# Kernel tuning notes

Hardware: AMD Instinct MI355X
Metric: run time of the kernel (lower is better)

## Reference

```python
import jax, jax.numpy as jnp
import numpy as np

N6 = 524288          # nodes at depth 6 (full-octree batch of 2)
N5 = N6 // 8         # 65536 nodes at depth 5
N4 = N5 // 8         # 8192 nodes at depth 4
EPS = 1e-5           # torch BatchNorm1d default eps


def _pool(x):
    # octree_max_pool on a full octree: 8 contiguous children -> parent max
    n, c = x.shape
    return jnp.max(x.reshape(n // 8, 8, c), axis=1)


def _up(x):
    # octree_upsample on a full octree: each parent broadcast to its 8 children
    return jnp.repeat(x, 8, axis=0)


def _conv1x1_bn_relu(x, w, g, b):
    # Conv1x1 (Linear, no bias) + BatchNorm1d (training-mode batch stats) + ReLU
    y = x @ w                              # [N, Cout]
    m = jnp.mean(y, axis=0)
    v = jnp.var(y, axis=0)                 # biased variance, as in torch BN
    y = (y - m) * jax.lax.rsqrt(v + EPS) * g + b
    return jax.nn.relu(y)


def setup_inputs() -> dict:
    key = jax.random.key(0)
    ks = jax.random.split(key, 8)
    s = 0.02
    return {
        "data0": jax.random.normal(ks[0], (N6, 96), jnp.float32),
        "data1": jax.random.normal(ks[1], (N5, 192), jnp.float32),
        "w01": jax.random.normal(ks[2], (96, 192), jnp.float32) * s,
        "g01": jnp.ones((192,), jnp.float32),
        "b01": jnp.zeros((192,), jnp.float32),
        "w02": jax.random.normal(ks[3], (96, 384), jnp.float32) * s,
        "g02": jnp.ones((384,), jnp.float32),
        "b02": jnp.zeros((384,), jnp.float32),
        "w10": jax.random.normal(ks[4], (192, 96), jnp.float32) * s,
        "g10": jnp.ones((96,), jnp.float32),
        "b10": jnp.zeros((96,), jnp.float32),
        "w12": jax.random.normal(ks[5], (192, 384), jnp.float32) * s,
        "g12": jnp.ones((384,), jnp.float32),
        "b12": jnp.zeros((384,), jnp.float32),
        "depth": 6,
    }


def reference(data0, data1, w01, g01, b01, w02, g02, b02,
              w10, g10, b10, w12, g12, b12, depth):
    # channels = [96, 192, 384]; data0 at depth, data1 at depth-1.
    # out[j] = sum_i TransFunc(channels[i]->channels[j])(data[i], depth-i -> depth-j)
    # j=0 (depth, 96ch):   identity(data0) + upsample(conv10(data1))
    out0 = data0 + _up(_conv1x1_bn_relu(data1, w10, g10, b10))
    # j=1 (depth-1, 192ch): conv01(pool(data0)) + identity(data1)
    p0 = _pool(data0)                      # [N5, 96]
    out1 = _conv1x1_bn_relu(p0, w01, g01, b01) + data1
    # j=2 (depth-2, 384ch): conv02(pool^2(data0)) + conv12(pool(data1))
    out2 = (_conv1x1_bn_relu(_pool(p0), w02, g02, b02)
            + _conv1x1_bn_relu(_pool(data1), w12, g12, b12))
    return (out0, out1, out2)
```

## Files before the change

### kernel.cpp

```cpp
#include <hip/hip_runtime.h>

typedef unsigned short u16;
typedef __attribute__((ext_vector_type(8))) short short8;
typedef __attribute__((ext_vector_type(4))) float f4;
typedef __attribute__((ext_vector_type(4))) unsigned short u16x4;

#define CN6 524288
#define CN5 65536
#define CN4 8192

__device__ inline u16 f2bf(float f){
  unsigned u = __float_as_uint(f);
  return (u16)((u + 0x7FFFu + ((u >> 16) & 1u)) >> 16);
}
__device__ inline float bf2f(u16 h){ return __uint_as_float(((unsigned)h) << 16); }

__device__ inline f4 nt_load4(const float* p){
  return __builtin_nontemporal_load(reinterpret_cast<const f4*>(p));
}
__device__ inline void nt_store4(float* p, f4 v){
  __builtin_nontemporal_store(v, reinterpret_cast<f4*>(p));
}


__global__ __launch_bounds__(256) void k_prep(const float* __restrict__ w10, const float* __restrict__ w01,
                                              const float* __restrict__ w02, const float* __restrict__ w12,
                                              u16* __restrict__ wT10, u16* __restrict__ wT01,
                                              u16* __restrict__ wT02, u16* __restrict__ wT12,
                                              float* __restrict__ stats){
  int i = blockIdx.x * 256 + threadIdx.x;
  if (i < 2112) stats[i] = 0.f;
  if (i < 18432){ int j = i / 192, k = i - j * 192; wT10[i] = f2bf(w10[k * 96 + j]); }
  else if (i < 36864){ int e = i - 18432; int j = e / 96, k = e - j * 96; wT01[e] = f2bf(w01[k * 192 + j]); }
  else if (i < 73728){ int e = i - 36864; int j = e / 96, k = e - j * 96; wT02[e] = f2bf(w02[k * 384 + j]); }
  else if (i < 147456){ int e = i - 73728; int j = e / 192, k = e - j * 192; wT12[e] = f2bf(w12[k * 384 + j]); }
}

__global__ __launch_bounds__(256) void k_gemm10p(const float* __restrict__ d1, const u16* __restrict__ wT10,
                                                 u16* __restrict__ y10, u16* __restrict__ p1){
  __shared__ u16 sm[32 * 200];
  int tid = threadIdx.x, bid = blockIdx.x;

  if (tid < 96){
    int p = tid / 24, c8 = tid - p * 24;
    f4 v0[8], v1[8];
    #pragma unroll
    for (int r = 0; r < 8; r++){
      const float* src = d1 + ((size_t)bid * 32 + p * 8 + r) * 192 + c8 * 8;
      v0[r] = *reinterpret_cast<const f4*>(src);
      v1[r] = *reinterpret_cast<const f4*>(src + 4);
    }
    float mx[8];
    #pragma unroll
    for (int q = 0; q < 4; q++){ mx[q] = v0[0][q]; mx[4 + q] = v1[0][q]; }
    #pragma unroll
    for (int r = 0; r < 8; r++){
      short8 h;
      #pragma unroll
      for (int q = 0; q < 4; q++){
        h[q]     = (short)f2bf(v0[r][q]);
        h[4 + q] = (short)f2bf(v1[r][q]);
        if (r){ mx[q] = fmaxf(mx[q], v0[r][q]); mx[4 + q] = fmaxf(mx[4 + q], v1[r][q]); }
      }
      *reinterpret_cast<short8*>(&sm[(p * 8 + r) * 200 + c8 * 8]) = h;
    }
    short8 hp;
    #pragma unroll
    for (int q = 0; q < 8; q++) hp[q] = (short)f2bf(mx[q]);
    *reinterpret_cast<short8*>(p1 + ((size_t)bid * 4 + p) * 192 + c8 * 8) = hp;
  }
  __syncthreads();

  int lane = tid & 63, wave = tid >> 6;
  int colb = lane & 15;
  int k0 = (lane >> 4) * 8, rgrp = (lane >> 4) * 4;
  int arowl = (wave & 1) * 16 + colb;
  int jbase = (wave >> 1) * 3;
  short8 xf[6];
  #pragma unroll
  for (int s = 0; s < 6; s++) xf[s] = *reinterpret_cast<short8*>(&sm[arowl * 200 + s * 32 + k0]);

  size_t xrow = (size_t)bid * 32 + arowl;
  #pragma unroll
  for (int jj = 0; jj < 3; jj++){
    int j = jbase + jj;
    f4 acc = {0.f, 0.f, 0.f, 0.f};
    const u16* wr = wT10 + (size_t)(j * 16 + colb) * 192 + k0;
    #pragma unroll
    for (int s = 0; s < 6; s++)
      acc = __builtin_amdgcn_mfma_f32_16x16x32_bf16(*reinterpret_cast<const short8*>(wr + s * 32), xf[s], acc, 0, 0, 0);
    u16x4 h;
    #pragma unroll
    for (int r = 0; r < 4; r++) h[r] = f2bf(acc[r]);
    *reinterpret_cast<u16x4*>(y10 + xrow * 96 + j * 16 + rgrp) = h;
  }
}

__global__ __launch_bounds__(192) void k_stats10(const u16* __restrict__ y10, float* __restrict__ stats){
  __shared__ float ls[96], lq[96];
  int tid = threadIdx.x, bid = blockIdx.x;
  if (tid < 96){ ls[tid] = 0.f; lq[tid] = 0.f; }
  __syncthreads();
  int c8 = tid % 12, rl = tid / 12;
  float s1[8], s2[8];
  #pragma unroll
  for (int q = 0; q < 8; q++){ s1[q] = 0.f; s2[q] = 0.f; }
  for (int it = 0; it < 32; it++){
    size_t row = (size_t)bid * 512 + it * 16 + rl;
    short8 h = *reinterpret_cast<const short8*>(y10 + row * 96 + c8 * 8);
    #pragma unroll
    for (int q = 0; q < 8; q++){
      float v = bf2f((u16)h[q]);
      s1[q] += v; s2[q] += v * v;
    }
  }
  #pragma unroll
  for (int q = 0; q < 8; q++){
    atomicAdd(&ls[c8 * 8 + q], s1[q]);
    atomicAdd(&lq[c8 * 8 + q], s2[q]);
  }
  __syncthreads();
  if (tid < 96){ atomicAdd(&stats[tid], ls[tid]); atomicAdd(&stats[1056 + tid], lq[tid]); }
}

__global__ __launch_bounds__(256) void k_out0(const float* __restrict__ d0, const u16* __restrict__ y10,
                                              const float* __restrict__ stats,
                                              const float* __restrict__ g10, const float* __restrict__ b10,
                                              float* __restrict__ out0, u16* __restrict__ p0, u16* __restrict__ p00){
  __shared__ float yv[8][96];
  __shared__ float sd[64][100];
  __shared__ float sp[8][96];
  int tid = threadIdx.x, gp = blockIdx.x;

  if (tid < 192){
    int p = tid / 24, c4 = tid - p * 24;
    u16x4 yb = *reinterpret_cast<const u16x4*>(y10 + ((size_t)gp * 8 + p) * 96 + c4 * 4);
    f4 o;
    #pragma unroll
    for (int q = 0; q < 4; q++){
      int c = c4 * 4 + q;
      float m = stats[c] * (1.f / 65536.f);
      float vv = stats[1056 + c] * (1.f / 65536.f) - m * m;
      float a = g10[c] * rsqrtf(vv + 1e-5f);
      float cc = b10[c] - m * a;
      o[q] = fmaxf(bf2f((u16)yb[q]) * a + cc, 0.f);
    }
    *reinterpret_cast<f4*>(&yv[p][c4 * 4]) = o;
  }
  __syncthreads();

  const float* dsrc = d0 + (size_t)gp * 6144;
  float* ddst = out0 + (size_t)gp * 6144;
  f4 v[6];
  #pragma unroll
  for (int i = 0; i < 6; i++) v[i] = nt_load4(dsrc + (i * 256 + tid) * 4);
  #pragma unroll
  for (int i = 0; i < 6; i++){
    int idx = i * 256 + tid;
    int row = idx / 24, c4 = idx - row * 24;
    f4 y = *reinterpret_cast<f4*>(&yv[row >> 3][c4 * 4]);
    f4 o;
    #pragma unroll
    for (int q = 0; q < 4; q++) o[q] = v[i][q] + y[q];
    nt_store4(ddst + idx * 4, o);
    *reinterpret_cast<f4*>(&sd[row][c4 * 4]) = v[i];
  }
  __syncthreads();

  if (tid < 192){
    int p = tid / 24, c4 = tid - p * 24;
    f4 m = *reinterpret_cast<f4*>(&sd[p * 8][c4 * 4]);
    #pragma unroll
    for (int r = 1; r < 8; r++){
      f4 x = *reinterpret_cast<f4*>(&sd[p * 8 + r][c4 * 4]);
      #pragma unroll
      for (int q = 0; q < 4; q++) m[q] = fmaxf(m[q], x[q]);
    }
    u16x4 h;
    #pragma unroll
    for (int q = 0; q < 4; q++) h[q] = f2bf(m[q]);
    *reinterpret_cast<u16x4*>(p0 + ((size_t)gp * 8 + p) * 96 + c4 * 4) = h;
    *reinterpret_cast<f4*>(&sp[p][c4 * 4]) = m;
  }
  __syncthreads();
  if (tid < 24){
    f4 m = *reinterpret_cast<f4*>(&sp[0][tid * 4]);
    #pragma unroll
    for (int pp = 1; pp < 8; pp++){
      f4 x = *reinterpret_cast<f4*>(&sp[pp][tid * 4]);
      #pragma unroll
      for (int q = 0; q < 4; q++) m[q] = fmaxf(m[q], x[q]);
    }
    u16x4 h;
    #pragma unroll
    for (int q = 0; q < 4; q++) h[q] = f2bf(m[q]);
    *reinterpret_cast<u16x4*>(p00 + (size_t)gp * 96 + tid * 4) = h;
  }
}

template<int Ci, int Co>
__device__ __forceinline__ void stats_body(const u16* __restrict__ x, const u16* __restrict__ wT,
                                           float* __restrict__ sum, float* __restrict__ sq,
                                           int bid, float* ls, float* lq){
  int tid = threadIdx.x;
  for (int t = tid; t < Co; t += 256){ ls[t] = 0.f; lq[t] = 0.f; }
  __syncthreads();
  int lane = tid & 63, wave = tid >> 6;
  int arow = bid * 64 + wave * 16 + (lane & 15);
  int k0 = (lane >> 4) * 8;
  constexpr int KS = Ci / 32;
  short8 af[KS];
  const u16* xr = x + (size_t)arow * Ci + k0;
  #pragma unroll
  for (int s = 0; s < KS; s++) af[s] = *reinterpret_cast<const short8*>(xr + s * 32);
  int colb = lane & 15;
  #pragma unroll 4
  for (int j = 0; j < Co / 16; j++){
    int col = j * 16 + colb;
    f4 acc = {0.f, 0.f, 0.f, 0.f};
    const u16* wr = wT + (size_t)col * Ci + k0;
    #pragma unroll
    for (int s = 0; s < KS; s++)
      acc = __builtin_amdgcn_mfma_f32_16x16x32_bf16(af[s], *reinterpret_cast<const short8*>(wr + s * 32), acc, 0, 0, 0);
    float s1 = acc[0] + acc[1] + acc[2] + acc[3];
    float s2 = acc[0]*acc[0] + acc[1]*acc[1] + acc[2]*acc[2] + acc[3]*acc[3];
    atomicAdd(&ls[col], s1);
    atomicAdd(&lq[col], s2);
  }
  __syncthreads();
  for (int t = tid; t < Co; t += 256){ atomicAdd(&sum[t], ls[t]); atomicAdd(&sq[t], lq[t]); }
}

__global__ __launch_bounds__(256) void k_statsAll(const u16* __restrict__ p0, const u16* __restrict__ p00,
                                                  const u16* __restrict__ p1,
                                                  const u16* __restrict__ wT01, const u16* __restrict__ wT02,
                                                  const u16* __restrict__ wT12, float* __restrict__ stats){
  __shared__ float ls[384], lq[384];
  int bid = blockIdx.x;
  if (bid < 1024)      stats_body<96, 192>(p0,  wT01, stats + 96,  stats + 1056 + 96,  bid,        ls, lq);
  else if (bid < 1152) stats_body<96, 384>(p00, wT02, stats + 288, stats + 1056 + 288, bid - 1024, ls, lq);
  else                 stats_body<192,384>(p1,  wT12, stats + 672, stats + 1056 + 672, bid - 1152, ls, lq);
}

__global__ __launch_bounds__(256) void k_out1(const u16* __restrict__ p0, const u16* __restrict__ wT01,
                                              const float* __restrict__ d1, const float* __restrict__ stats,
                                              const float* __restrict__ g01, const float* __restrict__ b01,
                                              float* __restrict__ out1){
  __shared__ float aL[192], cL[192];
  __shared__ float so[32 * 196];
  int tid = threadIdx.x, bid = blockIdx.x;
  if (tid < 192){
    float m = stats[96 + tid] * (1.f / 65536.f);
    float v = stats[1056 + 96 + tid] * (1.f / 65536.f) - m * m;
    float a = g01[tid] * rsqrtf(v + 1e-5f);
    aL[tid] = a; cL[tid] = b01[tid] - m * a;
  }
  __syncthreads();
  int lane = tid & 63, wave = tid >> 6;
  int colb = lane & 15;
  int k0 = (lane >> 4) * 8, rgrp = (lane >> 4) * 4;
  int rowl = (wave & 1) * 16 + colb;
  int jbase = (wave >> 1) * 6;
  short8 xf[3];
  const u16* xr = p0 + ((size_t)bid * 32 + rowl) * 96 + k0;
  #pragma unroll
  for (int s = 0; s < 3; s++) xf[s] = *reinterpret_cast<const short8*>(xr + s * 32);
  #pragma unroll
  for (int jj = 0; jj < 6; jj++){
    int j = jbase + jj;
    int ch0 = j * 16 + rgrp;
    f4 acc = {0.f, 0.f, 0.f, 0.f};
    const u16* wr = wT01 + (size_t)(j * 16 + colb) * 96 + k0;
    #pragma unroll
    for (int s = 0; s < 3; s++)
      acc = __builtin_amdgcn_mfma_f32_16x16x32_bf16(*reinterpret_cast<const short8*>(wr + s * 32), xf[s], acc, 0, 0, 0);
    f4 o;
    #pragma unroll
    for (int r = 0; r < 4; r++){
      int ch = ch0 + r;
      o[r] = fmaxf(acc[r] * aL[ch] + cL[ch], 0.f);
    }
    *reinterpret_cast<f4*>(&so[rowl * 196 + ch0]) = o;
  }
  __syncthreads();
  const float* d1b = d1 + (size_t)bid * 32 * 192;
  float* o1b = out1 + (size_t)bid * 32 * 192;
  #pragma unroll
  for (int i = 0; i < 6; i++){
    int idx = i * 256 + tid;
    int rl = idx / 48, c4i = idx % 48;
    f4 y = *reinterpret_cast<f4*>(&so[rl * 196 + c4i * 4]);
    int off = rl * 192 + c4i * 4;
    f4 g = nt_load4(d1b + off);
    f4 o;
    #pragma unroll
    for (int q = 0; q < 4; q++) o[q] = y[q] + g[q];
    nt_store4(o1b + off, o);
  }
}

__global__ __launch_bounds__(256) void k_out2(const u16* __restrict__ p00, const u16* __restrict__ p1,
                                              const u16* __restrict__ wT02, const u16* __restrict__ wT12,
                                              const float* __restrict__ stats,
                                              const float* __restrict__ g02, const float* __restrict__ b02,
                                              const float* __restrict__ g12, const float* __restrict__ b12,
                                              float* __restrict__ out2){
  __shared__ float a2[384], c2[384], a1[384], c1[384];
  __shared__ float so[32 * 392];
  int tid = threadIdx.x, bid = blockIdx.x;
  for (int t = tid; t < 384; t += 256){
    float m = stats[288 + t] * (1.f / 8192.f);
    float v = stats[1056 + 288 + t] * (1.f / 8192.f) - m * m;
    float a = g02[t] * rsqrtf(v + 1e-5f);
    a2[t] = a; c2[t] = b02[t] - m * a;
    m = stats[672 + t] * (1.f / 8192.f);
    v = stats[1056 + 672 + t] * (1.f / 8192.f) - m * m;
    a = g12[t] * rsqrtf(v + 1e-5f);
    a1[t] = a; c1[t] = b12[t] - m * a;
  }
  __syncthreads();
  int lane = tid & 63, wave = tid >> 6;
  int wr2 = wave >> 1, wc = wave & 1;
  int colb = lane & 15;
  int k0 = (lane >> 4) * 8, rgrp = (lane >> 4) * 4;
  int rowl = wr2 * 16 + colb;
  size_t arow = (size_t)bid * 32 + rowl;
  short8 xA[3], xB[6];
  #pragma unroll
  for (int s = 0; s < 3; s++) xA[s] = *reinterpret_cast<const short8*>(p00 + arow * 96 + k0 + s * 32);
  #pragma unroll
  for (int s = 0; s < 6; s++) xB[s] = *reinterpret_cast<const short8*>(p1 + arow * 192 + k0 + s * 32);
  #pragma unroll 2
  for (int j = 0; j < 12; j++){
    int ch0 = wc * 192 + j * 16 + rgrp;
    int wrow = wc * 192 + j * 16 + colb;
    f4 u = {0.f, 0.f, 0.f, 0.f}, w = {0.f, 0.f, 0.f, 0.f};
    const u16* wra = wT02 + (size_t)wrow * 96 + k0;
    #pragma unroll
    for (int s = 0; s < 3; s++)
      u = __builtin_amdgcn_mfma_f32_16x16x32_bf16(*reinterpret_cast<const short8*>(wra + s * 32), xA[s], u, 0, 0, 0);
    const u16* wrb = wT12 + (size_t)wrow * 192 + k0;
    #pragma unroll
    for (int s = 0; s < 6; s++)
      w = __builtin_amdgcn_mfma_f32_16x16x32_bf16(*reinterpret_cast<const short8*>(wrb + s * 32), xB[s], w, 0, 0, 0);
    f4 o;
    #pragma unroll
    for (int r = 0; r < 4; r++){
      int ch = ch0 + r;
      o[r] = fmaxf(u[r] * a2[ch] + c2[ch], 0.f) + fmaxf(w[r] * a1[ch] + c1[ch], 0.f);
    }
    *reinterpret_cast<f4*>(&so[rowl * 392 + ch0]) = o;
  }
  __syncthreads();
  #pragma unroll
  for (int i = 0; i < 12; i++){
    int idx = i * 256 + tid;
    int rl = idx / 96, c4i = idx % 96;
    f4 v = *reinterpret_cast<f4*>(&so[rl * 392 + c4i * 4]);
    nt_store4(out2 + ((size_t)bid * 32 + rl) * 384 + c4i * 4, v);
  }
}

extern "C" void kernel_launch(void* const* d_in, const int* in_sizes, int n_in,
                              void* d_out, int out_size, void* d_ws, size_t ws_size,
                              hipStream_t stream){
  const float* data0 = (const float*)d_in[0];
  const float* data1 = (const float*)d_in[1];
  const float* w01 = (const float*)d_in[2];
  const float* g01 = (const float*)d_in[3];
  const float* b01 = (const float*)d_in[4];
  const float* w02 = (const float*)d_in[5];
  const float* g02 = (const float*)d_in[6];
  const float* b02 = (const float*)d_in[7];
  const float* w10 = (const float*)d_in[8];
  const float* g10 = (const float*)d_in[9];
  const float* b10 = (const float*)d_in[10];
  const float* w12 = (const float*)d_in[11];
  const float* g12 = (const float*)d_in[12];
  const float* b12 = (const float*)d_in[13];

  float* out0 = (float*)d_out;
  float* out1 = out0 + (size_t)CN6 * 96;
  float* out2 = out1 + (size_t)CN5 * 192;

  char* ws = (char*)d_ws;
  u16* p1   = (u16*)(ws + 0);
  u16* p0   = (u16*)(ws + 3145728);
  u16* p00  = (u16*)(ws + 15728640);
  u16* y10  = (u16*)(ws + 17301504);
  u16* wT10 = (u16*)(ws + 29884416);
  u16* wT01 = (u16*)(ws + 29921280);
  u16* wT02 = (u16*)(ws + 29958144);
  u16* wT12 = (u16*)(ws + 30031872);
  float* stats = (float*)(ws + 30179328);

  k_prep<<<576, 256, 0, stream>>>(w10, w01, w02, w12, wT10, wT01, wT02, wT12, stats);
  k_gemm10p<<<2048, 256, 0, stream>>>(data1, wT10, y10, p1);
  k_stats10<<<128, 192, 0, stream>>>(y10, stats);
  k_out0<<<8192, 256, 0, stream>>>(data0, y10, stats, g10, b10, out0, p0, p00);
  k_statsAll<<<1280, 256, 0, stream>>>(p0, p00, p1, wT01, wT02, wT12, stats);
  k_out1<<<2048, 256, 0, stream>>>(p0, wT01, data1, stats, g01, b01, out1);
  k_out2<<<256, 256, 0, stream>>>(p00, p1, wT02, wT12, stats, g02, b02, g12, b12, out2);
}
```

Baseline: 213.2 us.

## Materialize conv01 output once in bf16 instead of recomputing GEMM for stats and output

```diff
diff --git a/kernel.cpp b/kernel.cpp
--- a/kernel.cpp
+++ b/kernel.cpp
@@ -198,6 +198,94 @@
   }
 }
 
+__global__ __launch_bounds__(256) void k_gemm01p(const u16* __restrict__ p0, const u16* __restrict__ wT01,
+                                                 u16* __restrict__ y01){
+  int tid = threadIdx.x, bid = blockIdx.x;
+  int lane = tid & 63, wave = tid >> 6;
+  int colb = lane & 15;
+  int k0 = (lane >> 4) * 8, rgrp = (lane >> 4) * 4;
+  int rowl = (wave & 1) * 16 + colb;
+  int jbase = (wave >> 1) * 6;
+  short8 xf[3];
+  const u16* xr = p0 + ((size_t)bid * 32 + rowl) * 96 + k0;
+  #pragma unroll
+  for (int s = 0; s < 3; s++) xf[s] = *reinterpret_cast<const short8*>(xr + s * 32);
+  size_t xrow = (size_t)bid * 32 + rowl;
+  #pragma unroll
+  for (int jj = 0; jj < 6; jj++){
+    int j = jbase + jj;
+    f4 acc = {0.f, 0.f, 0.f, 0.f};
+    const u16* wr = wT01 + (size_t)(j * 16 + colb) * 96 + k0;
+    #pragma unroll
+    for (int s = 0; s < 3; s++)
+      acc = __builtin_amdgcn_mfma_f32_16x16x32_bf16(*reinterpret_cast<const short8*>(wr + s * 32), xf[s], acc, 0, 0, 0);
+    u16x4 h;
+    #pragma unroll
+    for (int r = 0; r < 4; r++) h[r] = f2bf(acc[r]);
+    *reinterpret_cast<u16x4*>(y01 + xrow * 192 + j * 16 + rgrp) = h;
+  }
+}
+
+__global__ __launch_bounds__(192) void k_stats01(const u16* __restrict__ y01, float* __restrict__ stats){
+  __shared__ float ls[192], lq[192];
+  int tid = threadIdx.x, bid = blockIdx.x;
+  ls[tid] = 0.f; lq[tid] = 0.f;
+  __syncthreads();
+  int c8 = tid % 24, rl = tid / 24;
+  float s1[8], s2[8];
+  #pragma unroll
+  for (int q = 0; q < 8; q++){ s1[q] = 0.f; s2[q] = 0.f; }
+  for (int it = 0; it < 64; it++){
+    size_t row = (size_t)bid * 512 + it * 8 + rl;
+    short8 h = *reinterpret_cast<const short8*>(y01 + row * 192 + c8 * 8);
+    #pragma unroll
+    for (int q = 0; q < 8; q++){
+      float v = bf2f((u16)h[q]);
+      s1[q] += v; s2[q] += v * v;
+    }
+  }
+  #pragma unroll
+  for (int q = 0; q < 8; q++){
+    atomicAdd(&ls[c8 * 8 + q], s1[q]);
+    atomicAdd(&lq[c8 * 8 + q], s2[q]);
+  }
+  __syncthreads();
+  atomicAdd(&stats[96 + tid], ls[tid]);
+  atomicAdd(&stats[1056 + 96 + tid], lq[tid]);
+}
+
+__global__ __launch_bounds__(256) void k_out1lite(const u16* __restrict__ y01, const float* __restrict__ d1,
+                                                  const float* __restrict__ stats,
+                                                  const float* __restrict__ g01, const float* __restrict__ b01,
+                                                  float* __restrict__ out1){
+  __shared__ float aL[192], cL[192];
+  int tid = threadIdx.x, bid = blockIdx.x;
+  if (tid < 192){
+    float m = stats[96 + tid] * (1.f / 65536.f);
+    float v = stats[1056 + 96 + tid] * (1.f / 65536.f) - m * m;
+    float a = g01[tid] * rsqrtf(v + 1e-5f);
+    aL[tid] = a; cL[tid] = b01[tid] - m * a;
+  }
+  __syncthreads();
+  const u16* yb = y01 + (size_t)bid * 64 * 192;
+  const float* d1b = d1 + (size_t)bid * 64 * 192;
+  float* o1b = out1 + (size_t)bid * 64 * 192;
+  #pragma unroll
+  for (int i = 0; i < 12; i++){
+    int idx = i * 256 + tid;
+    int c4i = idx % 48;
+    u16x4 yv = *reinterpret_cast<const u16x4*>(yb + idx * 4);
+    f4 g = nt_load4(d1b + idx * 4);
+    f4 o;
+    #pragma unroll
+    for (int q = 0; q < 4; q++){
+      int ch = c4i * 4 + q;
+      o[q] = fmaxf(bf2f((u16)yv[q]) * aL[ch] + cL[ch], 0.f) + g[q];
+    }
+    nt_store4(o1b + idx * 4, o);
+  }
+}
+
 template<int Ci, int Co>
 __device__ __forceinline__ void stats_body(const u16* __restrict__ x, const u16* __restrict__ wT,
                                            float* __restrict__ sum, float* __restrict__ sq,
@@ -231,72 +319,13 @@
   for (int t = tid; t < Co; t += 256){ atomicAdd(&sum[t], ls[t]); atomicAdd(&sq[t], lq[t]); }
 }
 
-__global__ __launch_bounds__(256) void k_statsAll(const u16* __restrict__ p0, const u16* __restrict__ p00,
-                                                  const u16* __restrict__ p1,
-                                                  const u16* __restrict__ wT01, const u16* __restrict__ wT02,
-                                                  const u16* __restrict__ wT12, float* __restrict__ stats){
+__global__ __launch_bounds__(256) void k_statsAll(const u16* __restrict__ p00, const u16* __restrict__ p1,
+                                                  const u16* __restrict__ wT02, const u16* __restrict__ wT12,
+                                                  float* __restrict__ stats){
   __shared__ float ls[384], lq[384];
   int bid = blockIdx.x;
-  if (bid < 1024)      stats_body<96, 192>(p0,  wT01, stats + 96,  stats + 1056 + 96,  bid,        ls, lq);
-  else if (bid < 1152) stats_body<96, 384>(p00, wT02, stats + 288, stats + 1056 + 288, bid - 1024, ls, lq);
-  else                 stats_body<192,384>(p1,  wT12, stats + 672, stats + 1056 + 672, bid - 1152, ls, lq);
-}
-
-__global__ __launch_bounds__(256) void k_out1(const u16* __restrict__ p0, const u16* __restrict__ wT01,
-                                              const float* __restrict__ d1, const float* __restrict__ stats,
-                                              const float* __restrict__ g01, const float* __restrict__ b01,
-                                              float* __restrict__ out1){
-  __shared__ float aL[192], cL[192];
-  __shared__ float so[32 * 196];
-  int tid = threadIdx.x, bid = blockIdx.x;
-  if (tid < 192){
-    float m = stats[96 + tid] * (1.f / 65536.f);
-    float v = stats[1056 + 96 + tid] * (1.f / 65536.f) - m * m;
-    float a = g01[tid] * rsqrtf(v + 1e-5f);
-    aL[tid] = a; cL[tid] = b01[tid] - m * a;
-  }
-  __syncthreads();
-  int lane = tid & 63, wave = tid >> 6;
-  int colb = lane & 15;
-  int k0 = (lane >> 4) * 8, rgrp = (lane >> 4) * 4;
-  int rowl = (wave & 1) * 16 + colb;
-  int jbase = (wave >> 1) * 6;
-  short8 xf[3];
-  const u16* xr = p0 + ((size_t)bid * 32 + rowl) * 96 + k0;
-  #pragma unroll
-  for (int s = 0; s < 3; s++) xf[s] = *reinterpret_cast<const short8*>(xr + s * 32);
-  #pragma unroll
-  for (int jj = 0; jj < 6; jj++){
-    int j = jbase + jj;
-    int ch0 = j * 16 + rgrp;
-    f4 acc = {0.f, 0.f, 0.f, 0.f};
-    const u16* wr = wT01 + (size_t)(j * 16 + colb) * 96 + k0;
-    #pragma unroll
-    for (int s = 0; s < 3; s++)
-      acc = __builtin_amdgcn_mfma_f32_16x16x32_bf16(*reinterpret_cast<const short8*>(wr + s * 32), xf[s], acc, 0, 0, 0);
-    f4 o;
-    #pragma unroll
-    for (int r = 0; r < 4; r++){
-      int ch = ch0 + r;
-      o[r] = fmaxf(acc[r] * aL[ch] + cL[ch], 0.f);
-    }
-    *reinterpret_cast<f4*>(&so[rowl * 196 + ch0]) = o;
-  }
-  __syncthreads();
-  const float* d1b = d1 + (size_t)bid * 32 * 192;
-  float* o1b = out1 + (size_t)bid * 32 * 192;
-  #pragma unroll
-  for (int i = 0; i < 6; i++){
-    int idx = i * 256 + tid;
-    int rl = idx / 48, c4i = idx % 48;
-    f4 y = *reinterpret_cast<f4*>(&so[rl * 196 + c4i * 4]);
-    int off = rl * 192 + c4i * 4;
-    f4 g = nt_load4(d1b + off);
-    f4 o;
-    #pragma unroll
-    for (int q = 0; q < 4; q++) o[q] = y[q] + g[q];
-    nt_store4(o1b + off, o);
-  }
+  if (bid < 128) stats_body<96, 384>(p00, wT02, stats + 288, stats + 1056 + 288, bid,       ls, lq);
+  else           stats_body<192,384>(p1,  wT12, stats + 672, stats + 1056 + 672, bid - 128, ls, lq);
 }
 
 __global__ __launch_bounds__(256) void k_out2(const u16* __restrict__ p00, const u16* __restrict__ p1,
@@ -393,12 +422,15 @@
   u16* wT02 = (u16*)(ws + 29958144);
   u16* wT12 = (u16*)(ws + 30031872);
   float* stats = (float*)(ws + 30179328);
+  u16* y01  = (u16*)(ws + 30187776);
 
   k_prep<<<576, 256, 0, stream>>>(w10, w01, w02, w12, wT10, wT01, wT02, wT12, stats);
   k_gemm10p<<<2048, 256, 0, stream>>>(data1, wT10, y10, p1);
   k_stats10<<<128, 192, 0, stream>>>(y10, stats);
   k_out0<<<8192, 256, 0, stream>>>(data0, y10, stats, g10, b10, out0, p0, p00);
-  k_statsAll<<<1280, 256, 0, stream>>>(p0, p00, p1, wT01, wT02, wT12, stats);
-  k_out1<<<2048, 256, 0, stream>>>(p0, wT01, data1, stats, g01, b01, out1);
+  k_gemm01p<<<2048, 256, 0, stream>>>(p0, wT01, y01);
+  k_stats01<<<128, 192, 0, stream>>>(y01, stats);
+  k_statsAll<<<256, 256, 0, stream>>>(p00, p1, wT02, wT12, stats);
+  k_out1lite<<<1024, 256, 0, stream>>>(y01, data1, stats, g01, b01, out1);
   k_out2<<<256, 256, 0, stream>>>(p00, p1, wT02, wT12, stats, g02, b02, g12, b12, out2);
 }
```

New measurement: 215.1 us. About the same (+0.9%).
